# Kernel optimization log

Measured on AMD Instinct MI355X. Metric: run time of the kernel, lower is better.

## Reference

```python
import jax, jax.numpy as jnp
import numpy as np

T_END = 100.0  # observation window length


def setup_inputs() -> dict:
    key = jax.random.key(0)
    k1, k2, k3, k4, k5 = jax.random.split(key, 5)
    B, N, num_type, num_decay = 4, 2048, 50, 4
    # sorted event times in [0, T_END)
    event_times = jnp.sort(jax.random.uniform(k1, (B, N), dtype=jnp.float32) * T_END, axis=-1)
    event_types = jax.random.randint(k2, (B, N), 0, num_type)
    input_mask = jnp.ones((B, N), dtype=jnp.float32)
    t0 = jnp.zeros((B,), dtype=jnp.float32)
    t1 = jnp.full((B,), T_END, dtype=jnp.float32)
    # raw (pre-softplus) parameters, as in torch init
    mu_p = jax.random.normal(k3, (num_type,), dtype=jnp.float32) * 0.5 - 2.0
    alpha_p = jax.random.normal(k4, (num_type, num_type, num_decay), dtype=jnp.float32) * 0.5 - 3.0
    beta_p = jax.random.normal(k5, (num_decay,), dtype=jnp.float32) * 0.5 - 3.0
    return {"event_times": event_times, "event_types": event_types,
            "input_mask": input_mask, "t0": t0, "t1": t1,
            "mu_p": mu_p, "alpha_p": alpha_p, "beta_p": beta_p}


def reference(event_times, event_types, input_mask, t0, t1, mu_p, alpha_p, beta_p):
    B, N = event_times.shape
    mhat = jax.nn.softplus(mu_p)            # [T]
    Ahat = jax.nn.softplus(alpha_p)         # [T, T, D]
    omega = jax.nn.softplus(beta_p)         # [D]

    mu = mhat[event_types]                  # [B, N]
    # pairwise time differences, strictly-lower-triangular (i > j) kept
    dt = event_times[:, :, None] - event_times[:, None, :]     # [B, N, N]
    tril = jnp.tril(jnp.ones((N, N), dtype=bool), k=-1)        # strict lower
    dt = jnp.where(tril, dt, 0.0)
    # decay kernel per decay component: [B, D, N, N]
    kern = omega[None, :, None, None] * jnp.exp(-omega[None, :, None, None] * dt[:, None])
    # gather excitation matrix entries by (type_i, type_j): [B, N, N, D] -> [B, D, N, N]
    Auu = Ahat[event_types[:, :, None], event_types[:, None, :]]
    Auu = jnp.transpose(Auu, (0, 3, 1, 2))
    ag = jnp.where(tril[None, None], Auu * kern, 0.0)           # tril(diagonal=-1)
    rates = mu + ag.sum(axis=(1, 3))                            # [B, N]

    compensator_baseline = (t1 - t0) * jnp.sum(mhat)            # [B]
    # integrated kernel: [B, D, N]
    log_kernel = -omega[None, :, None] * (t1[:, None] - event_times)[:, None, :]
    Int_kernel = 1.0 - jnp.exp(log_kernel)
    # Ahat[:, event_types]: [T, B, N, D] -> permute to [B, T, D, N]
    Au = jnp.transpose(Ahat[:, event_types], (1, 0, 3, 2))
    Au_Int = (Au * Int_kernel[:, None]).sum(axis=1).sum(axis=1) * input_mask  # [B, N]
    compensator = compensator_baseline + Au_Int.sum(axis=1)     # [B]

    loglik = (jnp.log(rates + 1e-8) * input_mask).sum(axis=-1)  # [B]
    return (loglik, compensator)
```

## Files before the change

kernel.cpp:

```cpp
#include <hip/hip_runtime.h>
#include <math.h>

#define NT 50
#define ND 4
#define NB 4
#define NN 2048
#define TI 32
#define SUBS 8
#define TILES (NN/TI)
#define GRID (NB*TILES)

__device__ __forceinline__ float softplus_stable(float x) {
    return fmaxf(x, 0.0f) + log1pf(__expf(-fabsf(x)));
}

__global__ __launch_bounds__(256) void hawkes_kernel(
        const float* __restrict__ times,
        const int*   __restrict__ types,
        const float* __restrict__ mask,
        const float* __restrict__ t0v,
        const float* __restrict__ t1v,
        const float* __restrict__ mu_p,
        const float* __restrict__ alpha_p,
        const float* __restrict__ beta_p,
        float* __restrict__ out) {
    __shared__ float4 At4[NT * NT];
    __shared__ float4 S4[NT];
    __shared__ float4 cls4[NT];
    __shared__ float4 E4s[TI];
    __shared__ int    ctile[TI];
    __shared__ float  wls[4];
    __shared__ float  redA[8];

    int t     = threadIdx.x;
    int b     = blockIdx.x >> 6;
    int k     = blockIdx.x & 63;
    int tile0 = k * TI;
    int base  = b * NN;
    int il    = t >> 3;
    int sub   = t & 7;
    int i     = tile0 + il;
    int e     = base + i;

    if (t < ND) wls[t] = softplus_stable(beta_p[t]);
    if (t < NT) S4[t] = make_float4(0.f, 0.f, 0.f, 0.f);
    __syncthreads();
    float w0 = wls[0], w1 = wls[1], w2 = wls[2], w3 = wls[3];
    float T0 = times[base + tile0];

    for (int q = t; q < NT * NT; q += 256) {
        float4 a = ((const float4*)alpha_p)[q];
        a.x = softplus_stable(a.x); a.y = softplus_stable(a.y);
        a.z = softplus_stable(a.z); a.w = softplus_stable(a.w);
        int ty = q / NT, c = q - ty * NT;
        At4[c * NT + ty] = a;
    }
    for (int j = t; j < tile0; j += 256) {
        float tj = times[base + j];
        int   cj = types[base + j];
        float dt = tj - T0;
        float* sp = (float*)&S4[cj];
        atomicAdd(sp + 0, __expf(w0 * dt));
        atomicAdd(sp + 1, __expf(w1 * dt));
        atomicAdd(sp + 2, __expf(w2 * dt));
        atomicAdd(sp + 3, __expf(w3 * dt));
    }
    if (t < TI) {
        int j = tile0 + t;
        float dt = times[base + j] - T0;
        E4s[t] = make_float4(__expf(w0 * dt), __expf(w1 * dt),
                             __expf(w2 * dt), __expf(w3 * dt));
        ctile[t] = types[base + j] * NT;
    }
    __syncthreads();

    if (t < NT * ND) {
        int c = t >> 2, d = t & 3;
        const float* col = (const float*)&At4[c * NT];
        float s = 0.f;
        for (int ty = 0; ty < NT; ++ty) s += col[ty * 4 + d];
        ((float*)&cls4[c])[d] = s;
    }

    float ti_ = times[e];
    int   ty  = types[e];
    float ddt = ti_ - T0;
    float F0 = __expf(-w0 * ddt), F1 = __expf(-w1 * ddt);
    float F2 = __expf(-w2 * ddt), F3 = __expf(-w3 * ddt);

    float a0 = 0.f, a1 = 0.f, a2 = 0.f, a3 = 0.f;
    if (tile0 > 0) {
        for (int c = sub; c < NT; c += SUBS) {
            float4 A = At4[c * NT + ty];
            float4 S = S4[c];
            a0 = fmaf(A.x, S.x, a0); a1 = fmaf(A.y, S.y, a1);
            a2 = fmaf(A.z, S.z, a2); a3 = fmaf(A.w, S.w, a3);
        }
    }
    for (int jj = sub; jj < il; jj += SUBS) {
        float4 A = At4[ctile[jj] + ty];
        float4 E = E4s[jj];
        a0 = fmaf(A.x, E.x, a0); a1 = fmaf(A.y, E.y, a1);
        a2 = fmaf(A.z, E.z, a2); a3 = fmaf(A.w, E.w, a3);
    }
    float p = w0 * F0 * a0 + w1 * F1 * a1 + w2 * F2 * a2 + w3 * F3 * a3;
    p += __shfl_xor(p, 1, 64);
    p += __shfl_xor(p, 2, 64);
    p += __shfl_xor(p, 4, 64);
    __syncthreads();

    float ll = 0.f, cp = 0.f;
    if (sub == 0) {
        float mk   = mask[e];
        float rate = softplus_stable(mu_p[ty]) + p;
        ll = logf(rate + 1e-8f) * mk;
        float tt = t1v[b] - ti_;
        float4 cs = cls4[ty];
        cp = (cs.x * (1.f - __expf(-w0 * tt)) + cs.y * (1.f - __expf(-w1 * tt)) +
              cs.z * (1.f - __expf(-w2 * tt)) + cs.w * (1.f - __expf(-w3 * tt))) * mk;
    }
    #pragma unroll
    for (int off = 8; off < 64; off <<= 1) {
        ll += __shfl_xor(ll, off, 64);
        cp += __shfl_xor(cp, off, 64);
    }
    int lane = t & 63, wid = t >> 6;
    if (lane == 0) { redA[wid] = ll; redA[4 + wid] = cp; }
    __syncthreads();
    if (t == 0) {
        atomicAdd(&out[b],      redA[0] + redA[1] + redA[2] + redA[3]);
        atomicAdd(&out[NB + b], redA[4] + redA[5] + redA[6] + redA[7]);
    }
    if (k == 0 && t < 64) {
        float sp = (t < NT) ? softplus_stable(mu_p[t]) : 0.f;
        #pragma unroll
        for (int off = 32; off > 0; off >>= 1) sp += __shfl_down(sp, off, 64);
        if (t == 0) atomicAdd(&out[NB + b], (t1v[b] - t0v[b]) * sp);
    }
}

extern "C" void kernel_launch(void* const* d_in, const int* in_sizes, int n_in,
                              void* d_out, int out_size, void* d_ws, size_t ws_size,
                              hipStream_t stream) {
    const float* times   = (const float*)d_in[0];
    const int*   types   = (const int*)  d_in[1];
    const float* mask    = (const float*)d_in[2];
    const float* t0      = (const float*)d_in[3];
    const float* t1      = (const float*)d_in[4];
    const float* mu_p    = (const float*)d_in[5];
    const float* alpha_p = (const float*)d_in[6];
    const float* beta_p  = (const float*)d_in[7];
    float* out = (float*)d_out;

    hipMemsetAsync(out, 0, 2 * NB * sizeof(float), stream);
    hawkes_kernel<<<GRID, 256, 0, stream>>>(times, types, mask, t0, t1,
                                            mu_p, alpha_p, beta_p, out);
}
```

Before: 90.96 us.

## Precompute softplus of alpha and column sums in a prep kernel via workspace

Adds a small prep kernel that applies softplus to the alpha tensor once, computes the per-column type sums, zeroes the output and adds the baseline compensator. This replaces the hipMemsetAsync and stops every one of the 256 main blocks from redoing 10000 softplus evaluations and a column-sum pass. The main kernel now copies the preprocessed alpha into shared memory untransposed and indexes it row-wise. It also drops one barrier by moving the sync earlier. The cost is an extra kernel launch and a dependency on the workspace buffer.

```diff
diff --git a/kernel.cpp b/kernel.cpp
--- a/kernel.cpp
+++ b/kernel.cpp
@@ -9,24 +9,59 @@
 #define SUBS 8
 #define TILES (NN/TI)
 #define GRID (NB*TILES)
+#define OFF_CLS 10000
 
 __device__ __forceinline__ float softplus_stable(float x) {
     return fmaxf(x, 0.0f) + log1pf(__expf(-fabsf(x)));
+}
+
+__global__ __launch_bounds__(256) void prep_kernel(
+        const float* __restrict__ alpha_p,
+        const float* __restrict__ mu_p,
+        const float* __restrict__ t0v,
+        const float* __restrict__ t1v,
+        float* __restrict__ ws,
+        float* __restrict__ out) {
+    int t = threadIdx.x;
+    int g = blockIdx.x * 256 + t;
+    if (g < NT * NT) {
+        float4 a = ((const float4*)alpha_p)[g];
+        a.x = softplus_stable(a.x); a.y = softplus_stable(a.y);
+        a.z = softplus_stable(a.z); a.w = softplus_stable(a.w);
+        ((float4*)ws)[g] = a;
+    }
+    if (blockIdx.x == 0) {
+        if (t < 2 * NB) out[t] = 0.0f;
+        if (t < NT * ND) {
+            float s = 0.0f;
+            for (int kk = 0; kk < NT; ++kk)
+                s += softplus_stable(alpha_p[kk * (NT * ND) + t]);
+            ws[OFF_CLS + t] = s;
+        }
+        __syncthreads();
+        if (t < 64) {
+            float sp = (t < NT) ? softplus_stable(mu_p[t]) : 0.0f;
+            #pragma unroll
+            for (int off = 32; off > 0; off >>= 1) sp += __shfl_down(sp, off, 64);
+            if (t == 0) {
+                for (int b = 0; b < NB; ++b)
+                    out[NB + b] += (t1v[b] - t0v[b]) * sp;
+            }
+        }
+    }
 }
 
 __global__ __launch_bounds__(256) void hawkes_kernel(
         const float* __restrict__ times,
         const int*   __restrict__ types,
         const float* __restrict__ mask,
-        const float* __restrict__ t0v,
         const float* __restrict__ t1v,
         const float* __restrict__ mu_p,
-        const float* __restrict__ alpha_p,
         const float* __restrict__ beta_p,
+        const float* __restrict__ ws,
         float* __restrict__ out) {
     __shared__ float4 At4[NT * NT];
     __shared__ float4 S4[NT];
-    __shared__ float4 cls4[NT];
     __shared__ float4 E4s[TI];
     __shared__ int    ctile[TI];
     __shared__ float  wls[4];
@@ -48,17 +83,13 @@
     float w0 = wls[0], w1 = wls[1], w2 = wls[2], w3 = wls[3];
     float T0 = times[base + tile0];
 
-    for (int q = t; q < NT * NT; q += 256) {
-        float4 a = ((const float4*)alpha_p)[q];
-        a.x = softplus_stable(a.x); a.y = softplus_stable(a.y);
-        a.z = softplus_stable(a.z); a.w = softplus_stable(a.w);
-        int ty = q / NT, c = q - ty * NT;
-        At4[c * NT + ty] = a;
-    }
+    #pragma unroll 2
+    for (int q = t; q < NT * NT; q += 256)
+        At4[q] = ((const float4*)ws)[q];
+
     for (int j = t; j < tile0; j += 256) {
-        float tj = times[base + j];
+        float dt = times[base + j] - T0;
         int   cj = types[base + j];
-        float dt = tj - T0;
         float* sp = (float*)&S4[cj];
         atomicAdd(sp + 0, __expf(w0 * dt));
         atomicAdd(sp + 1, __expf(w1 * dt));
@@ -70,16 +101,7 @@
         float dt = times[base + j] - T0;
         E4s[t] = make_float4(__expf(w0 * dt), __expf(w1 * dt),
                              __expf(w2 * dt), __expf(w3 * dt));
-        ctile[t] = types[base + j] * NT;
-    }
-    __syncthreads();
-
-    if (t < NT * ND) {
-        int c = t >> 2, d = t & 3;
-        const float* col = (const float*)&At4[c * NT];
-        float s = 0.f;
-        for (int ty = 0; ty < NT; ++ty) s += col[ty * 4 + d];
-        ((float*)&cls4[c])[d] = s;
+        ctile[t] = types[base + j];
     }
 
     float ti_ = times[e];
@@ -87,18 +109,20 @@
     float ddt = ti_ - T0;
     float F0 = __expf(-w0 * ddt), F1 = __expf(-w1 * ddt);
     float F2 = __expf(-w2 * ddt), F3 = __expf(-w3 * ddt);
+    __syncthreads();
 
+    int tyNT = ty * NT;
     float a0 = 0.f, a1 = 0.f, a2 = 0.f, a3 = 0.f;
     if (tile0 > 0) {
         for (int c = sub; c < NT; c += SUBS) {
-            float4 A = At4[c * NT + ty];
+            float4 A = At4[tyNT + c];
             float4 S = S4[c];
             a0 = fmaf(A.x, S.x, a0); a1 = fmaf(A.y, S.y, a1);
             a2 = fmaf(A.z, S.z, a2); a3 = fmaf(A.w, S.w, a3);
         }
     }
     for (int jj = sub; jj < il; jj += SUBS) {
-        float4 A = At4[ctile[jj] + ty];
+        float4 A = At4[tyNT + ctile[jj]];
         float4 E = E4s[jj];
         a0 = fmaf(A.x, E.x, a0); a1 = fmaf(A.y, E.y, a1);
         a2 = fmaf(A.z, E.z, a2); a3 = fmaf(A.w, E.w, a3);
@@ -107,7 +131,6 @@
     p += __shfl_xor(p, 1, 64);
     p += __shfl_xor(p, 2, 64);
     p += __shfl_xor(p, 4, 64);
-    __syncthreads();
 
     float ll = 0.f, cp = 0.f;
     if (sub == 0) {
@@ -115,7 +138,7 @@
         float rate = softplus_stable(mu_p[ty]) + p;
         ll = logf(rate + 1e-8f) * mk;
         float tt = t1v[b] - ti_;
-        float4 cs = cls4[ty];
+        float4 cs = ((const float4*)(ws + OFF_CLS))[ty];
         cp = (cs.x * (1.f - __expf(-w0 * tt)) + cs.y * (1.f - __expf(-w1 * tt)) +
               cs.z * (1.f - __expf(-w2 * tt)) + cs.w * (1.f - __expf(-w3 * tt))) * mk;
     }
@@ -131,12 +154,6 @@
         atomicAdd(&out[b],      redA[0] + redA[1] + redA[2] + redA[3]);
         atomicAdd(&out[NB + b], redA[4] + redA[5] + redA[6] + redA[7]);
     }
-    if (k == 0 && t < 64) {
-        float sp = (t < NT) ? softplus_stable(mu_p[t]) : 0.f;
-        #pragma unroll
-        for (int off = 32; off > 0; off >>= 1) sp += __shfl_down(sp, off, 64);
-        if (t == 0) atomicAdd(&out[NB + b], (t1v[b] - t0v[b]) * sp);
-    }
 }
 
 extern "C" void kernel_launch(void* const* d_in, const int* in_sizes, int n_in,
@@ -151,8 +168,9 @@
     const float* alpha_p = (const float*)d_in[6];
     const float* beta_p  = (const float*)d_in[7];
     float* out = (float*)d_out;
+    float* ws  = (float*)d_ws;
 
-    hipMemsetAsync(out, 0, 2 * NB * sizeof(float), stream);
-    hawkes_kernel<<<GRID, 256, 0, stream>>>(times, types, mask, t0, t1,
-                                            mu_p, alpha_p, beta_p, out);
+    prep_kernel<<<10, 256, 0, stream>>>(alpha_p, mu_p, t0, t1, ws, out);
+    hawkes_kernel<<<GRID, 256, 0, stream>>>(times, types, mask, t1,
+                                            mu_p, beta_p, ws, out);
 }
```

New measurement: 106.7 us. 17.3% more time.

## Replace memset with cooperative launch and grid sync for output init

Applied to the files above, without the earlier changes.

Drops the separate hipMemsetAsync. Block 0 now initializes the outputs, writing the baseline compensator into them directly, and a cooperative grid sync orders that initialization before every block's atomic accumulation. The shared alpha matrix is also stored in its natural row-major layout, so the per-event gathers index by the event's own type row instead of by column. Column sums are moved after a single barrier. The cost is a grid-wide barrier and the extra overhead of a cooperative launch, in exchange for removing one stream operation.

```diff
diff --git a/kernel.cpp b/kernel.cpp
--- a/kernel.cpp
+++ b/kernel.cpp
@@ -1,5 +1,8 @@
 #include <hip/hip_runtime.h>
+#include <hip/hip_cooperative_groups.h>
 #include <math.h>
+
+namespace cg = cooperative_groups;
 
 #define NT 50
 #define ND 4
@@ -14,7 +17,7 @@
     return fmaxf(x, 0.0f) + log1pf(__expf(-fabsf(x)));
 }
 
-__global__ __launch_bounds__(256) void hawkes_kernel(
+__global__ __launch_bounds__(256) void hawkes_all(
         const float* __restrict__ times,
         const int*   __restrict__ types,
         const float* __restrict__ mask,
@@ -39,11 +42,24 @@
     int base  = b * NN;
     int il    = t >> 3;
     int sub   = t & 7;
-    int i     = tile0 + il;
-    int e     = base + i;
+    int e     = base + tile0 + il;
 
     if (t < ND) wls[t] = softplus_stable(beta_p[t]);
     if (t < NT) S4[t] = make_float4(0.f, 0.f, 0.f, 0.f);
+
+    if (blockIdx.x == 0 && t < 64) {
+        float sp = (t < NT) ? softplus_stable(mu_p[t]) : 0.f;
+        #pragma unroll
+        for (int off = 32; off > 0; off >>= 1) sp += __shfl_down(sp, off, 64);
+        if (t == 0) {
+            #pragma unroll
+            for (int bb = 0; bb < NB; ++bb) {
+                out[bb]      = 0.f;
+                out[NB + bb] = (t1v[bb] - t0v[bb]) * sp;
+            }
+            __threadfence();
+        }
+    }
     __syncthreads();
     float w0 = wls[0], w1 = wls[1], w2 = wls[2], w3 = wls[3];
     float T0 = times[base + tile0];
@@ -52,13 +68,11 @@
         float4 a = ((const float4*)alpha_p)[q];
         a.x = softplus_stable(a.x); a.y = softplus_stable(a.y);
         a.z = softplus_stable(a.z); a.w = softplus_stable(a.w);
-        int ty = q / NT, c = q - ty * NT;
-        At4[c * NT + ty] = a;
+        At4[q] = a;
     }
     for (int j = t; j < tile0; j += 256) {
-        float tj = times[base + j];
+        float dt = times[base + j] - T0;
         int   cj = types[base + j];
-        float dt = tj - T0;
         float* sp = (float*)&S4[cj];
         atomicAdd(sp + 0, __expf(w0 * dt));
         atomicAdd(sp + 1, __expf(w1 * dt));
@@ -70,35 +84,35 @@
         float dt = times[base + j] - T0;
         E4s[t] = make_float4(__expf(w0 * dt), __expf(w1 * dt),
                              __expf(w2 * dt), __expf(w3 * dt));
-        ctile[t] = types[base + j] * NT;
+        ctile[t] = types[base + j];
     }
-    __syncthreads();
-
-    if (t < NT * ND) {
-        int c = t >> 2, d = t & 3;
-        const float* col = (const float*)&At4[c * NT];
-        float s = 0.f;
-        for (int ty = 0; ty < NT; ++ty) s += col[ty * 4 + d];
-        ((float*)&cls4[c])[d] = s;
-    }
-
     float ti_ = times[e];
     int   ty  = types[e];
     float ddt = ti_ - T0;
     float F0 = __expf(-w0 * ddt), F1 = __expf(-w1 * ddt);
     float F2 = __expf(-w2 * ddt), F3 = __expf(-w3 * ddt);
+    __syncthreads();
 
+    if (t < NT * ND) {
+        int c = t >> 2, d = t & 3;
+        const float* Af = (const float*)At4;
+        float s = 0.f;
+        for (int yy = 0; yy < NT; ++yy) s += Af[yy * (NT * 4) + c * 4 + d];
+        ((float*)&cls4[c])[d] = s;
+    }
+
+    int tyNT = ty * NT;
     float a0 = 0.f, a1 = 0.f, a2 = 0.f, a3 = 0.f;
     if (tile0 > 0) {
         for (int c = sub; c < NT; c += SUBS) {
-            float4 A = At4[c * NT + ty];
+            float4 A = At4[tyNT + c];
             float4 S = S4[c];
             a0 = fmaf(A.x, S.x, a0); a1 = fmaf(A.y, S.y, a1);
             a2 = fmaf(A.z, S.z, a2); a3 = fmaf(A.w, S.w, a3);
         }
     }
     for (int jj = sub; jj < il; jj += SUBS) {
-        float4 A = At4[ctile[jj] + ty];
+        float4 A = At4[tyNT + ctile[jj]];
         float4 E = E4s[jj];
         a0 = fmaf(A.x, E.x, a0); a1 = fmaf(A.y, E.y, a1);
         a2 = fmaf(A.z, E.z, a2); a3 = fmaf(A.w, E.w, a3);
@@ -127,15 +141,18 @@
     int lane = t & 63, wid = t >> 6;
     if (lane == 0) { redA[wid] = ll; redA[4 + wid] = cp; }
     __syncthreads();
+
+    float outll = 0.f, outcp = 0.f;
     if (t == 0) {
-        atomicAdd(&out[b],      redA[0] + redA[1] + redA[2] + redA[3]);
-        atomicAdd(&out[NB + b], redA[4] + redA[5] + redA[6] + redA[7]);
+        outll = redA[0] + redA[1] + redA[2] + redA[3];
+        outcp = redA[4] + redA[5] + redA[6] + redA[7];
     }
-    if (k == 0 && t < 64) {
-        float sp = (t < NT) ? softplus_stable(mu_p[t]) : 0.f;
-        #pragma unroll
-        for (int off = 32; off > 0; off >>= 1) sp += __shfl_down(sp, off, 64);
-        if (t == 0) atomicAdd(&out[NB + b], (t1v[b] - t0v[b]) * sp);
+
+    cg::this_grid().sync();
+
+    if (t == 0) {
+        atomicAdd(&out[b],      outll);
+        atomicAdd(&out[NB + b], outcp);
     }
 }
 
@@ -152,7 +169,9 @@
     const float* beta_p  = (const float*)d_in[7];
     float* out = (float*)d_out;
 
-    hipMemsetAsync(out, 0, 2 * NB * sizeof(float), stream);
-    hawkes_kernel<<<GRID, 256, 0, stream>>>(times, types, mask, t0, t1,
-                                            mu_p, alpha_p, beta_p, out);
+    void* args[] = { (void*)&times, (void*)&types, (void*)&mask, (void*)&t0,
+                     (void*)&t1, (void*)&mu_p, (void*)&alpha_p, (void*)&beta_p,
+                     (void*)&out };
+    hipLaunchCooperativeKernel((const void*)hawkes_all, dim3(GRID), dim3(256),
+                               args, 0, stream);
 }
```

Measured after the change: 149.0 us. 1.64x slower.
